# Performance work log

Hardware: AMD Instinct MI355X
Metric: run time of the kernel (lower is better)

Reference implementation:

```python
import jax, jax.numpy as jnp
import numpy as np

N_VARS = 10
TOPK = 30  # max(1, int(100 * 0.3))


def get_adjacency(W_logits):
    W = jax.nn.sigmoid(W_logits)
    W = W * (1.0 - jnp.eye(N_VARS, dtype=W.dtype))
    flat = W.reshape(-1)
    topv, _ = jax.lax.top_k(flat, TOPK)
    threshold = topv[-1]
    mask = (W >= threshold).astype(W.dtype)
    return W * mask


def setup_inputs() -> dict:
    key = jax.random.key(0)
    ks = jax.random.split(key, 9)
    B = 500000
    X = jax.random.normal(ks[0], (B, N_VARS), dtype=jnp.float32)
    # learned soft-adjacency logits (nonzero so the top-k mask is non-trivial)
    W_logits = jax.random.normal(ks[1], (N_VARS, N_VARS), dtype=jnp.float32)
    # stacked per-node MLP params: j indexes the 10 node-specific MLPs
    s1 = 1.0 / np.sqrt(10.0)
    s2 = 1.0 / np.sqrt(64.0)
    s3 = 1.0 / np.sqrt(32.0)
    W1 = jax.random.uniform(ks[2], (N_VARS, 64, 10), jnp.float32, -s1, s1)
    b1 = jax.random.uniform(ks[3], (N_VARS, 64), jnp.float32, -s1, s1)
    W2 = jax.random.uniform(ks[4], (N_VARS, 32, 64), jnp.float32, -s2, s2)
    b2 = jax.random.uniform(ks[5], (N_VARS, 32), jnp.float32, -s2, s2)
    W3 = jax.random.uniform(ks[6], (N_VARS, 32), jnp.float32, -s3, s3)
    b3 = jax.random.uniform(ks[7], (N_VARS,), jnp.float32, -s3, s3)
    return {"X": X, "W_logits": W_logits, "W1": W1, "b1": b1,
            "W2": W2, "b2": b2, "W3": W3, "b3": b3}


def reference(X, W_logits, W1, b1, W2, b2, W3, b3):
    W = get_adjacency(W_logits)  # [10, 10]
    # xj[b, j, i] = X[b, i] * W[i, j]  (column-j mask of features for MLP j)
    xj = X[:, None, :] * W.T[None, :, :]           # [B, 10, 10]
    h1 = jnp.einsum('bji,jhi->bjh', xj, W1) + b1   # [B, 10, 64]
    h1 = jax.nn.gelu(h1, approximate=False)
    h2 = jnp.einsum('bjh,joh->bjo', h1, W2) + b2   # [B, 10, 32]
    h2 = jax.nn.gelu(h2, approximate=False)
    X_hat = jnp.einsum('bjo,jo->bj', h2, W3) + b3  # [B, 10]
    return X_hat, W
```

## Files before the change

### kernel.cpp

```cpp
#include <hip/hip_runtime.h>
#include <hip/hip_bf16.h>
#include <math.h>

#define NV  10
#define H1  64
#define H2  32

typedef __attribute__((ext_vector_type(8))) short bf16x8;
typedef __attribute__((ext_vector_type(4))) float f32x4;
typedef __attribute__((ext_vector_type(4))) unsigned int u32x4;

union frag_u { bf16x8 f; u32x4 u; unsigned int w[4]; };

#define MFMA(a,b,c) __builtin_amdgcn_mfma_f32_16x16x32_bf16(a, b, c, 0, 0, 0)

__device__ __forceinline__ unsigned short f2bf(float f) {
    union { __hip_bfloat16 h; unsigned short u; } cv;
    cv.h = __float2bfloat16(f);
    return cv.u;
}
__device__ __forceinline__ unsigned int pack2(float lo, float hi) {
    return (unsigned)f2bf(lo) | ((unsigned)f2bf(hi) << 16);
}

__device__ __forceinline__ float gelu_poly(float x) {
    float p  = __builtin_amdgcn_fmed3f(x, -3.0f, 3.0f);
    float p2 = p * p;
    float t  = __builtin_fmaf(p2, -4.6113e-6f,    1.47439e-4f);
    t        = __builtin_fmaf(p2, t, -2.136050e-3f);
    t        = __builtin_fmaf(p2, t,  1.966256e-2f);
    t        = __builtin_fmaf(p2, t, -1.3288786e-1f);
    t        = __builtin_fmaf(p2, t,  7.9788456e-1f);
    float P  = p * t;
    float hx = 0.5f * x;
    float y  = __builtin_fmaf(hx, P, hx);
    float big = fmaxf(x, 0.0f);
    return (__builtin_fabsf(x) > 3.0f) ? big : y;
}

__global__ void prep_W(const float* __restrict__ Wl,
                       const float* __restrict__ W1,
                       const float* __restrict__ b1,
                       const float* __restrict__ W2,
                       float* __restrict__ Wout,
                       unsigned short* __restrict__ a1,
                       unsigned short* __restrict__ a2) {
    __shared__ float W[100];
    __shared__ float thrv;
    int t = threadIdx.x;
    if (t < 100) {
        int i = t / NV, j = t % NV;
        float w = 1.0f / (1.0f + expf(-Wl[t]));
        if (i == j) w = 0.0f;
        W[t] = w;
    }
    __syncthreads();
    if (t < 100) {
        float v = W[t];
        int cnt = 0;
        #pragma unroll
        for (int k = 0; k < 100; ++k) cnt += (W[k] > v) ? 1 : 0;
        if (cnt == 29) thrv = v;
    }
    __syncthreads();
    if (t < 100) {
        float v = W[t];
        float m = (v >= thrv) ? v : 0.0f;
        Wout[t] = m;
        W[t] = m;
    }
    __syncthreads();
    for (int n = t; n < 20480; n += 256) {
        int b = n & 7, l = (n >> 3) & 63, tt = (n >> 9) & 3, j = n >> 11;
        int h = 16 * tt + (l & 15);
        int k = ((l >> 4) << 3) + b;
        float val = 0.0f;
        if (k < 10)       val = W1[j * 640 + h * 10 + k] * W[k * NV + j];
        else if (k == 10) val = b1[j * 64 + h];
        a1[n] = f2bf(val);
    }
    for (int n = t; n < 20480; n += 256) {
        int b = n & 7, l = (n >> 3) & 63, ks = (n >> 9) & 1, t2 = (n >> 10) & 1, j = n >> 11;
        int o = 16 * t2 + (l & 15);
        int h = 32 * ks + ((l >> 4) << 3) + b;
        a2[n] = f2bf(W2[j * 2048 + o * 64 + h]);
    }
}

__global__ __launch_bounds__(256, 4) void ncd_mfma(
    const float* __restrict__ X,
    const unsigned short* __restrict__ a1u,
    const unsigned short* __restrict__ a2u,
    const float* __restrict__ b2,
    const float* __restrict__ W3,
    const float* __restrict__ b3,
    float* __restrict__ out,
    int Bn, int ntiles)
{
    __shared__ float b2s[320];
    __shared__ float w3s[320];
    __shared__ unsigned xlds[4][512];

    for (int i = threadIdx.x; i < 320; i += 256) { b2s[i] = b2[i]; w3s[i] = W3[i]; }
    __syncthreads();

    const int wave = threadIdx.x >> 6;
    const int lane = threadIdx.x & 63;
    const int q = lane >> 4;
    const int s = lane & 15;
    const int tile = blockIdx.x * 4 + wave;
    if (tile >= ntiles) return;
    const int sbase = tile * 16;

    int row = sbase + s; if (row > Bn - 1) row = Bn - 1;
    const float* xr = X + (size_t)row * 10;
    frag_u xb;
    if (q == 0) {
        float2 v0 = *(const float2*)(xr + 0), v1 = *(const float2*)(xr + 2);
        float2 v2 = *(const float2*)(xr + 4), v3 = *(const float2*)(xr + 6);
        xb.w[0] = pack2(v0.x, v0.y); xb.w[1] = pack2(v1.x, v1.y);
        xb.w[2] = pack2(v2.x, v2.y); xb.w[3] = pack2(v3.x, v3.y);
    } else if (q == 1) {
        float2 v4 = *(const float2*)(xr + 8);
        xb.w[0] = pack2(v4.x, v4.y);
        xb.w[1] = pack2(1.0f, 0.0f);
        xb.w[2] = 0u; xb.w[3] = 0u;
    } else {
        xb.w[0] = xb.w[1] = xb.w[2] = xb.w[3] = 0u;
    }

    const bf16x8* A1 = (const bf16x8*)a1u;
    const bf16x8* A2 = (const bf16x8*)a2u;
    unsigned* wb = xlds[wave];
    const int sw = (s & 7) << 2;
    const f32x4 zf = {0.0f, 0.0f, 0.0f, 0.0f};

    #pragma unroll 1
    for (int j = 0; j < NV; ++j) {
        f32x4 acc[4];
        #pragma unroll
        for (int tt = 0; tt < 4; ++tt) {
            frag_u af; af.f = A1[(j * 4 + tt) * 64 + lane];
            acc[tt] = MFMA(af.f, xb.f, zf);
        }
        #pragma unroll
        for (int tt = 0; tt < 4; ++tt) {
            float g0 = gelu_poly(acc[tt][0]);
            float g1 = gelu_poly(acc[tt][1]);
            float g2 = gelu_poly(acc[tt][2]);
            float g3 = gelu_poly(acc[tt][3]);
            int w0 = 8 * tt + 2 * q;
            wb[s * 32 + ((w0    ) ^ sw)] = pack2(g0, g1);
            wb[s * 32 + ((w0 + 1) ^ sw)] = pack2(g2, g3);
        }
        f32x4 acc2[2] = {zf, zf};
        #pragma unroll
        for (int ks = 0; ks < 2; ++ks) {
            frag_u bf;
            bf.u = *(const u32x4*)&wb[s * 32 + ((16 * ks + 4 * q) ^ sw)];
            #pragma unroll
            for (int t2 = 0; t2 < 2; ++t2) {
                frag_u af; af.f = A2[((j * 2 + t2) * 2 + ks) * 64 + lane];
                acc2[t2] = MFMA(af.f, bf.f, acc2[t2]);
            }
        }
        float partial = 0.0f;
        #pragma unroll
        for (int t2 = 0; t2 < 2; ++t2) {
            float4 b2v = *(const float4*)&b2s[j * 32 + 16 * t2 + 4 * q];
            float4 w3v = *(const float4*)&w3s[j * 32 + 16 * t2 + 4 * q];
            partial += gelu_poly(acc2[t2][0] + b2v.x) * w3v.x;
            partial += gelu_poly(acc2[t2][1] + b2v.y) * w3v.y;
            partial += gelu_poly(acc2[t2][2] + b2v.z) * w3v.z;
            partial += gelu_poly(acc2[t2][3] + b2v.w) * w3v.w;
        }
        partial += __shfl_xor(partial, 16);
        partial += __shfl_xor(partial, 32);
        float rj = partial + b3[j];
        if (lane < 16 && sbase + lane < Bn) {
            out[(size_t)(sbase + lane) * 10 + j] = rj;
        }
    }
}

extern "C" void kernel_launch(void* const* d_in, const int* in_sizes, int n_in,
                              void* d_out, int out_size, void* d_ws, size_t ws_size,
                              hipStream_t stream) {
    const float* X  = (const float*)d_in[0];
    const float* Wl = (const float*)d_in[1];
    const float* W1 = (const float*)d_in[2];
    const float* b1 = (const float*)d_in[3];
    const float* W2 = (const float*)d_in[4];
    const float* b2 = (const float*)d_in[5];
    const float* W3 = (const float*)d_in[6];
    const float* b3 = (const float*)d_in[7];
    float* out = (float*)d_out;

    int B = in_sizes[0] / NV;
    float* Wout = out + (size_t)B * NV;
    unsigned short* a1 = (unsigned short*)d_ws;
    unsigned short* a2 = a1 + 20480;

    hipLaunchKernelGGL(prep_W, dim3(1), dim3(256), 0, stream,
                       Wl, W1, b1, W2, Wout, a1, a2);

    int ntiles = (B + 15) / 16;
    int blocks = (ntiles + 3) / 4;
    hipLaunchKernelGGL(ncd_mfma, dim3(blocks), dim3(256), 0, stream,
                       X, a1, a2, b2, W3, b3, out, B, ntiles);
}
```

Measured before the change: 208.2 us.

## Assign each wave a fixed node MLP and loop persistently over batch tiles

Each wave now owns a single node index j and walks batch tiles with a grid stride, instead of looping over all 10 nodes for one tile. The MFMA weight fragments, b2, W3 and b3 for that node are loaded into registers once, which removes the per-iteration global weight loads and the shared-memory staging of b2 and W3. The grid becomes a fixed persistent size of 2560 blocks. In exchange, each X row is now read and converted to bf16 ten times, by ten different waves. Output stores are also scattered per column, and the extra live registers may reduce occupancy.

```diff
diff --git a/kernel.cpp b/kernel.cpp
--- a/kernel.cpp
+++ b/kernel.cpp
@@ -95,54 +95,66 @@
     const float* __restrict__ W3,
     const float* __restrict__ b3,
     float* __restrict__ out,
-    int Bn, int ntiles)
+    int Bn, int ntiles, int jstride)
 {
-    __shared__ float b2s[320];
-    __shared__ float w3s[320];
     __shared__ unsigned xlds[4][512];
-
-    for (int i = threadIdx.x; i < 320; i += 256) { b2s[i] = b2[i]; w3s[i] = W3[i]; }
-    __syncthreads();
 
     const int wave = threadIdx.x >> 6;
     const int lane = threadIdx.x & 63;
     const int q = lane >> 4;
     const int s = lane & 15;
-    const int tile = blockIdx.x * 4 + wave;
-    if (tile >= ntiles) return;
-    const int sbase = tile * 16;
-
-    int row = sbase + s; if (row > Bn - 1) row = Bn - 1;
-    const float* xr = X + (size_t)row * 10;
-    frag_u xb;
-    if (q == 0) {
-        float2 v0 = *(const float2*)(xr + 0), v1 = *(const float2*)(xr + 2);
-        float2 v2 = *(const float2*)(xr + 4), v3 = *(const float2*)(xr + 6);
-        xb.w[0] = pack2(v0.x, v0.y); xb.w[1] = pack2(v1.x, v1.y);
-        xb.w[2] = pack2(v2.x, v2.y); xb.w[3] = pack2(v3.x, v3.y);
-    } else if (q == 1) {
-        float2 v4 = *(const float2*)(xr + 8);
-        xb.w[0] = pack2(v4.x, v4.y);
-        xb.w[1] = pack2(1.0f, 0.0f);
-        xb.w[2] = 0u; xb.w[3] = 0u;
-    } else {
-        xb.w[0] = xb.w[1] = xb.w[2] = xb.w[3] = 0u;
-    }
+
+    const int gw = blockIdx.x * 4 + wave;
+    const int j  = gw % NV;
+    const int t0 = gw / NV;
 
     const bf16x8* A1 = (const bf16x8*)a1u;
     const bf16x8* A2 = (const bf16x8*)a2u;
+    bf16x8 af1[4], af2[4];
+    #pragma unroll
+    for (int tt = 0; tt < 4; ++tt) af1[tt] = A1[(j * 4 + tt) * 64 + lane];
+    #pragma unroll
+    for (int t2 = 0; t2 < 2; ++t2)
+        #pragma unroll
+        for (int ks = 0; ks < 2; ++ks)
+            af2[t2 * 2 + ks] = A2[((j * 2 + t2) * 2 + ks) * 64 + lane];
+    float4 b2v[2], w3v[2];
+    #pragma unroll
+    for (int t2 = 0; t2 < 2; ++t2) {
+        b2v[t2] = *(const float4*)(b2 + j * 32 + 16 * t2 + 4 * q);
+        w3v[t2] = *(const float4*)(W3 + j * 32 + 16 * t2 + 4 * q);
+    }
+    const float b3j = b3[j];
+
     unsigned* wb = xlds[wave];
     const int sw = (s & 7) << 2;
     const f32x4 zf = {0.0f, 0.0f, 0.0f, 0.0f};
 
     #pragma unroll 1
-    for (int j = 0; j < NV; ++j) {
+    for (int tile = t0; tile < ntiles; tile += jstride) {
+        const int sbase = tile * 16;
+
+        int row = sbase + s; if (row > Bn - 1) row = Bn - 1;
+        const float* xr = X + (size_t)row * 10;
+        frag_u xb;
+        if (q == 0) {
+            float2 v0 = *(const float2*)(xr + 0), v1 = *(const float2*)(xr + 2);
+            float2 v2 = *(const float2*)(xr + 4), v3 = *(const float2*)(xr + 6);
+            xb.w[0] = pack2(v0.x, v0.y); xb.w[1] = pack2(v1.x, v1.y);
+            xb.w[2] = pack2(v2.x, v2.y); xb.w[3] = pack2(v3.x, v3.y);
+        } else if (q == 1) {
+            float2 v4 = *(const float2*)(xr + 8);
+            xb.w[0] = pack2(v4.x, v4.y);
+            xb.w[1] = pack2(1.0f, 0.0f);
+            xb.w[2] = 0u; xb.w[3] = 0u;
+        } else {
+            xb.w[0] = xb.w[1] = xb.w[2] = xb.w[3] = 0u;
+        }
+
         f32x4 acc[4];
         #pragma unroll
-        for (int tt = 0; tt < 4; ++tt) {
-            frag_u af; af.f = A1[(j * 4 + tt) * 64 + lane];
-            acc[tt] = MFMA(af.f, xb.f, zf);
-        }
+        for (int tt = 0; tt < 4; ++tt) acc[tt] = MFMA(af1[tt], xb.f, zf);
+
         #pragma unroll
         for (int tt = 0; tt < 4; ++tt) {
             float g0 = gelu_poly(acc[tt][0]);
@@ -153,30 +165,28 @@
             wb[s * 32 + ((w0    ) ^ sw)] = pack2(g0, g1);
             wb[s * 32 + ((w0 + 1) ^ sw)] = pack2(g2, g3);
         }
+
         f32x4 acc2[2] = {zf, zf};
         #pragma unroll
         for (int ks = 0; ks < 2; ++ks) {
-            frag_u bf;
-            bf.u = *(const u32x4*)&wb[s * 32 + ((16 * ks + 4 * q) ^ sw)];
+            frag_u bfg;
+            bfg.u = *(const u32x4*)&wb[s * 32 + ((16 * ks + 4 * q) ^ sw)];
             #pragma unroll
-            for (int t2 = 0; t2 < 2; ++t2) {
-                frag_u af; af.f = A2[((j * 2 + t2) * 2 + ks) * 64 + lane];
-                acc2[t2] = MFMA(af.f, bf.f, acc2[t2]);
-            }
-        }
+            for (int t2 = 0; t2 < 2; ++t2)
+                acc2[t2] = MFMA(af2[t2 * 2 + ks], bfg.f, acc2[t2]);
+        }
+
         float partial = 0.0f;
         #pragma unroll
         for (int t2 = 0; t2 < 2; ++t2) {
-            float4 b2v = *(const float4*)&b2s[j * 32 + 16 * t2 + 4 * q];
-            float4 w3v = *(const float4*)&w3s[j * 32 + 16 * t2 + 4 * q];
-            partial += gelu_poly(acc2[t2][0] + b2v.x) * w3v.x;
-            partial += gelu_poly(acc2[t2][1] + b2v.y) * w3v.y;
-            partial += gelu_poly(acc2[t2][2] + b2v.z) * w3v.z;
-            partial += gelu_poly(acc2[t2][3] + b2v.w) * w3v.w;
+            partial += gelu_poly(acc2[t2][0] + b2v[t2].x) * w3v[t2].x;
+            partial += gelu_poly(acc2[t2][1] + b2v[t2].y) * w3v[t2].y;
+            partial += gelu_poly(acc2[t2][2] + b2v[t2].z) * w3v[t2].z;
+            partial += gelu_poly(acc2[t2][3] + b2v[t2].w) * w3v[t2].w;
         }
         partial += __shfl_xor(partial, 16);
         partial += __shfl_xor(partial, 32);
-        float rj = partial + b3[j];
+        float rj = partial + b3j;
         if (lane < 16 && sbase + lane < Bn) {
             out[(size_t)(sbase + lane) * 10 + j] = rj;
         }
@@ -205,7 +215,8 @@
                        Wl, W1, b1, W2, Wout, a1, a2);
 
     int ntiles = (B + 15) / 16;
-    int blocks = (ntiles + 3) / 4;
+    const int blocks = 2560;
+    const int jstride = blocks * 4 / NV;
     hipLaunchKernelGGL(ncd_mfma, dim3(blocks), dim3(256), 0, stream,
-                       X, a1, a2, b2, W3, b3, out, B, ntiles);
-}
+                       X, a1, a2, b2, W3, b3, out, B, ntiles, jstride);
+}
```

Result: slower. 223.1 us (+7.2%).

## Feed layer-1 GELU outputs directly as MFMA B-operand, drop LDS round trip

Applied to the files above, without the earlier changes.

Permutes the packed W2 fragment layout so the k-index ordering matches how layer-1 accumulator outputs already sit in registers. Each lane then packs its GELU results straight into the B fragments for the second MFMA instead of writing to swizzled shared memory and reading back. This removes per-iteration LDS stores, loads and the associated latency and LDS allocation, relying on the reordered K dimension being consistent between the W2 prep and the register packing.

```diff
diff --git a/kernel.cpp b/kernel.cpp
--- a/kernel.cpp
+++ b/kernel.cpp
@@ -81,8 +81,10 @@
     }
     for (int n = t; n < 20480; n += 256) {
         int b = n & 7, l = (n >> 3) & 63, ks = (n >> 9) & 1, t2 = (n >> 10) & 1, j = n >> 11;
-        int o = 16 * t2 + (l & 15);
-        int h = 32 * ks + ((l >> 4) << 3) + b;
+        int o  = 16 * t2 + (l & 15);
+        int qk = l >> 4;
+        int hrel = (b < 4) ? (4 * qk + b) : (16 + 4 * qk + (b - 4));
+        int h  = 32 * ks + hrel;
         a2[n] = f2bf(W2[j * 2048 + o * 64 + h]);
     }
 }
@@ -99,8 +101,6 @@
 {
     __shared__ float b2s[320];
     __shared__ float w3s[320];
-    __shared__ unsigned xlds[4][512];
-
     for (int i = threadIdx.x; i < 320; i += 256) { b2s[i] = b2[i]; w3s[i] = W3[i]; }
     __syncthreads();
 
@@ -131,8 +131,6 @@
 
     const bf16x8* A1 = (const bf16x8*)a1u;
     const bf16x8* A2 = (const bf16x8*)a2u;
-    unsigned* wb = xlds[wave];
-    const int sw = (s & 7) << 2;
     const f32x4 zf = {0.0f, 0.0f, 0.0f, 0.0f};
 
     #pragma unroll 1
@@ -143,27 +141,29 @@
             frag_u af; af.f = A1[(j * 4 + tt) * 64 + lane];
             acc[tt] = MFMA(af.f, xb.f, zf);
         }
-        #pragma unroll
-        for (int tt = 0; tt < 4; ++tt) {
-            float g0 = gelu_poly(acc[tt][0]);
-            float g1 = gelu_poly(acc[tt][1]);
-            float g2 = gelu_poly(acc[tt][2]);
-            float g3 = gelu_poly(acc[tt][3]);
-            int w0 = 8 * tt + 2 * q;
-            wb[s * 32 + ((w0    ) ^ sw)] = pack2(g0, g1);
-            wb[s * 32 + ((w0 + 1) ^ sw)] = pack2(g2, g3);
-        }
+
+        frag_u pb0, pb1;
+        pb0.w[0] = pack2(gelu_poly(acc[0][0]), gelu_poly(acc[0][1]));
+        pb0.w[1] = pack2(gelu_poly(acc[0][2]), gelu_poly(acc[0][3]));
+        pb0.w[2] = pack2(gelu_poly(acc[1][0]), gelu_poly(acc[1][1]));
+        pb0.w[3] = pack2(gelu_poly(acc[1][2]), gelu_poly(acc[1][3]));
+        pb1.w[0] = pack2(gelu_poly(acc[2][0]), gelu_poly(acc[2][1]));
+        pb1.w[1] = pack2(gelu_poly(acc[2][2]), gelu_poly(acc[2][3]));
+        pb1.w[2] = pack2(gelu_poly(acc[3][0]), gelu_poly(acc[3][1]));
+        pb1.w[3] = pack2(gelu_poly(acc[3][2]), gelu_poly(acc[3][3]));
+
         f32x4 acc2[2] = {zf, zf};
         #pragma unroll
-        for (int ks = 0; ks < 2; ++ks) {
-            frag_u bf;
-            bf.u = *(const u32x4*)&wb[s * 32 + ((16 * ks + 4 * q) ^ sw)];
-            #pragma unroll
-            for (int t2 = 0; t2 < 2; ++t2) {
-                frag_u af; af.f = A2[((j * 2 + t2) * 2 + ks) * 64 + lane];
-                acc2[t2] = MFMA(af.f, bf.f, acc2[t2]);
-            }
-        }
+        for (int t2 = 0; t2 < 2; ++t2) {
+            frag_u af0; af0.f = A2[((j * 2 + t2) * 2 + 0) * 64 + lane];
+            acc2[t2] = MFMA(af0.f, pb0.f, acc2[t2]);
+        }
+        #pragma unroll
+        for (int t2 = 0; t2 < 2; ++t2) {
+            frag_u af1; af1.f = A2[((j * 2 + t2) * 2 + 1) * 64 + lane];
+            acc2[t2] = MFMA(af1.f, pb1.f, acc2[t2]);
+        }
+
         float partial = 0.0f;
         #pragma unroll
         for (int t2 = 0; t2 < 2; ++t2) {
```

After: 212.4 us. +2.0%, slower.
